# Kernel tuning notes

Hardware: AMD Instinct MI355X
Metric: run time of the kernel (lower is better)

The kernel has to match this reference:

```python
import jax, jax.numpy as jnp
import numpy as np


def setup_inputs() -> dict:
    key = jax.random.key(0)
    k_x, k_w, k_b = jax.random.split(key, 3)
    B, Cin, H, W = 32, 256, 56, 56
    Cout, KH, KW = 256, 3, 3
    x = jax.random.normal(k_x, (B, Cin, H, W), dtype=jnp.float32)
    fp_weight = jax.random.normal(k_w, (Cout, Cin, KH, KW), dtype=jnp.float32)
    # binary quantization, conv_mode='input_ch': per-output-channel scale
    scaling_factors = jnp.mean(jnp.abs(fp_weight), axis=(1, 2, 3), keepdims=True)  # [Cout,1,1,1]
    quant_weights = jnp.sign(fp_weight)  # values in {-1,0,1}
    bias = jax.random.normal(k_b, (Cout,), dtype=jnp.float32)
    return {"x": x, "scaling_factors": scaling_factors,
            "quant_weights": quant_weights, "bias": bias}


def reference(x, scaling_factors, quant_weights, bias):
    # Dequantize: per-out-channel scale times sign weights
    new_weights = scaling_factors * quant_weights  # [Cout,Cin,3,3]
    out = jax.lax.conv_general_dilated(
        x, new_weights,
        window_strides=(1, 1),
        padding=((1, 1), (1, 1)),
        dimension_numbers=("NCHW", "OIHW", "NCHW"),
    )
    return out + bias[None, :, None, None]
```

## Files before the change

### kernel.cpp

```cpp
#include <hip/hip_runtime.h>

using half8   = __attribute__((ext_vector_type(8))) _Float16;
using floatx4 = __attribute__((ext_vector_type(4))) float;
using floatx2 = __attribute__((ext_vector_type(2))) float;
using short8  = __attribute__((ext_vector_type(8))) short;

__global__ void repack_weights(const float* __restrict__ qw,
                               _Float16* __restrict__ wre, int n) {
  int t = blockIdx.x * 256 + threadIdx.x;
  if (t >= n) return;
  int c = t & 255, co = (t >> 8) & 255, s = t >> 16;
  wre[t] = (_Float16)qw[(co * 256 + c) * 9 + s];
}

__global__ __launch_bounds__(256, 2) void binconv_fused(
    const float* __restrict__ x, const float* __restrict__ scale,
    const float* __restrict__ bias, const _Float16* __restrict__ wre,
    float* __restrict__ out)
{
  __shared__ _Float16 xs[2 * 4 * 64 * 40];

  const int tid  = threadIdx.x;
  const int nb   = blockIdx.x;
  const int b    = nb / 28;
  const int h0   = (nb % 28) * 2;
  const int wave = tid >> 6;
  const int lane = tid & 63;
  const int nl   = lane & 15;
  const int quad = lane >> 4;
  const int co_wave = wave * 64;

  {
    short8 z = {0, 0, 0, 0, 0, 0, 0, 0};
    short8* xs8 = reinterpret_cast<short8*>(xs);
#pragma unroll
    for (int i = 0; i < 10; ++i) xs8[tid + i * 256] = z;
  }

  const int p   = lane & 15;
  const int wq  = lane >> 4;
  const int w0  = wq * 14;
  const int h   = h0 + wave - 1;
  const bool hok = (h >= 0) && (h < 56);
  const float* xca = x + (((size_t)b * 256 + 2 * p) * 56 + (hok ? h : 0)) * 56 + w0;
  const float* xcb = xca + 3136;
  _Float16* const wrow = xs + wave * 2560 + 2 * p;

  floatx2 va[7], vb[7];

  int bbase[7];
#pragma unroll
  for (int j = 0; j < 7; ++j) {
    int n = j * 16 + nl;
    int r = (n >= 56) ? 1 : 0;
    int w = n - r * 56;
    bbase[j] = (r * 64 + w) * 80 + quad * 16;
  }

  const _Float16* aptr[4];
#pragma unroll
  for (int mi = 0; mi < 4; ++mi)
    aptr[mi] = wre + (co_wave + mi * 16 + nl) * 256 + quad * 8;

  floatx4 acc[4][7];
#pragma unroll
  for (int mi = 0; mi < 4; ++mi)
#pragma unroll
    for (int j = 0; j < 7; ++j)
      acc[mi][j] = (floatx4){0.f, 0.f, 0.f, 0.f};

  __syncthreads();

  if (hok) {
#pragma unroll
    for (int i = 0; i < 7; ++i) {
      va[i] = *reinterpret_cast<const floatx2*>(xca + 2 * i);
      vb[i] = *reinterpret_cast<const floatx2*>(xcb + 2 * i);
    }
#pragma unroll
    for (int i = 0; i < 7; ++i) {
      auto u = __builtin_amdgcn_cvt_pkrtz(va[i][0], vb[i][0]);
      auto v = __builtin_amdgcn_cvt_pkrtz(va[i][1], vb[i][1]);
      *reinterpret_cast<decltype(u)*>(wrow + (w0 + 2 * i + 1) * 40) = u;
      *reinterpret_cast<decltype(v)*>(wrow + (w0 + 2 * i + 2) * 40) = v;
    }
  }

  int bufe = 0;
  for (int cc = 0; cc < 8; ++cc) {
    __syncthreads();
    if (cc < 7 && hok) {
      const float* A = xca + (size_t)(cc + 1) * 100352;
      const float* B = xcb + (size_t)(cc + 1) * 100352;
#pragma unroll
      for (int i = 0; i < 7; ++i) {
        va[i] = *reinterpret_cast<const floatx2*>(A + 2 * i);
        vb[i] = *reinterpret_cast<const floatx2*>(B + 2 * i);
      }
    }
    const int c0 = cc * 32;
    const char* xb = reinterpret_cast<const char*>(xs) + bufe * 2;
#pragma unroll
    for (int s = 0; s < 9; ++s) {
      const int kh = s / 3, kw = s - kh * 3;
      half8 a[4];
#pragma unroll
      for (int mi = 0; mi < 4; ++mi)
        a[mi] = *reinterpret_cast<const half8*>(aptr[mi] + s * 65536 + c0);
      const int soff = (kh * 64 + kw) * 80;
#pragma unroll
      for (int j = 0; j < 7; ++j) {
        half8 bf = *reinterpret_cast<const half8*>(xb + bbase[j] + soff);
#pragma unroll
        for (int mi = 0; mi < 4; ++mi)
          acc[mi][j] = __builtin_amdgcn_mfma_f32_16x16x32_f16(a[mi], bf, acc[mi][j], 0, 0, 0);
      }
    }
    if (cc < 7 && hok) {
      _Float16* d = wrow + (bufe ^ 10240);
#pragma unroll
      for (int i = 0; i < 7; ++i) {
        auto u = __builtin_amdgcn_cvt_pkrtz(va[i][0], vb[i][0]);
        auto v = __builtin_amdgcn_cvt_pkrtz(va[i][1], vb[i][1]);
        *reinterpret_cast<decltype(u)*>(d + (w0 + 2 * i + 1) * 40) = u;
        *reinterpret_cast<decltype(v)*>(d + (w0 + 2 * i + 2) * 40) = v;
      }
    }
    bufe ^= 10240;
  }

#pragma unroll
  for (int mi = 0; mi < 4; ++mi) {
#pragma unroll
    for (int reg = 0; reg < 4; ++reg) {
      int co = co_wave + mi * 16 + quad * 4 + reg;
      float s_ = scale[co];
      float bi = bias[co];
#pragma unroll
      for (int j = 0; j < 7; ++j) {
        int n = j * 16 + nl;
        int r = (n >= 56) ? 1 : 0;
        int w = n - r * 56;
        out[(((size_t)b * 256 + co) * 56 + (h0 + r)) * 56 + w] =
            acc[mi][j][reg] * s_ + bi;
      }
    }
  }
}

extern "C" void kernel_launch(void* const* d_in, const int* in_sizes, int n_in,
                              void* d_out, int out_size, void* d_ws, size_t ws_size,
                              hipStream_t stream) {
  const float* x     = (const float*)d_in[0];
  const float* scale = (const float*)d_in[1];
  const float* qw    = (const float*)d_in[2];
  const float* bias  = (const float*)d_in[3];
  float* out = (float*)d_out;

  _Float16* wre = (_Float16*)d_ws;

  repack_weights<<<2304, 256, 0, stream>>>(qw, wre, 9 * 256 * 256);
  binconv_fused<<<896, 256, 0, stream>>>(x, scale, bias, wre, out);
}
```

Baseline: 335.0 us.

## Split output channels across eight waves per block and raise MFMA priority

Doubles the block to 512 threads so each wave computes 32 output channels instead of 64. This halves the accumulator registers per wave and aims for more waves per CU to hide latency. The input staging is remapped so each thread loads one channel and writes scalar fp16 values into LDS instead of packed pairs. It also wraps the MFMA loop in s_setprio to favour the compute phase. The trade-off is that weight fragments are now reloaded by twice as many waves, LDS stores are narrower, and there is more synchronisation per block.

```diff
diff --git a/kernel.cpp b/kernel.cpp
--- a/kernel.cpp
+++ b/kernel.cpp
@@ -13,7 +13,7 @@
   wre[t] = (_Float16)qw[(co * 256 + c) * 9 + s];
 }
 
-__global__ __launch_bounds__(256, 2) void binconv_fused(
+__global__ __launch_bounds__(512, 4) void binconv_fused(
     const float* __restrict__ x, const float* __restrict__ scale,
     const float* __restrict__ bias, const _Float16* __restrict__ wre,
     float* __restrict__ out)
@@ -28,43 +28,45 @@
   const int lane = tid & 63;
   const int nl   = lane & 15;
   const int quad = lane >> 4;
-  const int co_wave = wave * 64;
+  const int co_wave = wave * 32;
 
   {
     short8 z = {0, 0, 0, 0, 0, 0, 0, 0};
     short8* xs8 = reinterpret_cast<short8*>(xs);
 #pragma unroll
-    for (int i = 0; i < 10; ++i) xs8[tid + i * 256] = z;
+    for (int i = 0; i < 5; ++i) xs8[tid + i * 512] = z;
   }
 
-  const int p   = lane & 15;
-  const int wq  = lane >> 4;
-  const int w0  = wq * 14;
-  const int h   = h0 + wave - 1;
-  const bool hok = (h >= 0) && (h < 56);
-  const float* xca = x + (((size_t)b * 256 + 2 * p) * 56 + (hok ? h : 0)) * 56 + w0;
-  const float* xcb = xca + 3136;
-  _Float16* const wrow = xs + wave * 2560 + 2 * p;
+  const int r     = wave >> 1;
+  const int chalf = wave & 1;
+  const int sc    = lane & 15;
+  const int q     = lane >> 4;
+  const int ch    = chalf * 16 + sc;
+  const int w0    = q * 14;
+  const int h     = h0 + r - 1;
+  const bool hok  = (h >= 0) && (h < 56);
+  const float* xc = x + (((size_t)b * 256 + ch) * 56 + (hok ? h : 0)) * 56 + w0;
+  _Float16* const wrow = xs + r * 2560 + ch;
 
-  floatx2 va[7], vb[7];
+  floatx2 va[7];
 
   int bbase[7];
 #pragma unroll
   for (int j = 0; j < 7; ++j) {
     int n = j * 16 + nl;
-    int r = (n >= 56) ? 1 : 0;
-    int w = n - r * 56;
-    bbase[j] = (r * 64 + w) * 80 + quad * 16;
+    int rr = (n >= 56) ? 1 : 0;
+    int w = n - rr * 56;
+    bbase[j] = (rr * 64 + w) * 80 + quad * 16;
   }
 
-  const _Float16* aptr[4];
+  const _Float16* aptr[2];
 #pragma unroll
-  for (int mi = 0; mi < 4; ++mi)
+  for (int mi = 0; mi < 2; ++mi)
     aptr[mi] = wre + (co_wave + mi * 16 + nl) * 256 + quad * 8;
 
-  floatx4 acc[4][7];
+  floatx4 acc[2][7];
 #pragma unroll
-  for (int mi = 0; mi < 4; ++mi)
+  for (int mi = 0; mi < 2; ++mi)
 #pragma unroll
     for (int j = 0; j < 7; ++j)
       acc[mi][j] = (floatx4){0.f, 0.f, 0.f, 0.f};
@@ -73,16 +75,12 @@
 
   if (hok) {
 #pragma unroll
-    for (int i = 0; i < 7; ++i) {
-      va[i] = *reinterpret_cast<const floatx2*>(xca + 2 * i);
-      vb[i] = *reinterpret_cast<const floatx2*>(xcb + 2 * i);
-    }
+    for (int i = 0; i < 7; ++i)
+      va[i] = *reinterpret_cast<const floatx2*>(xc + 2 * i);
 #pragma unroll
     for (int i = 0; i < 7; ++i) {
-      auto u = __builtin_amdgcn_cvt_pkrtz(va[i][0], vb[i][0]);
-      auto v = __builtin_amdgcn_cvt_pkrtz(va[i][1], vb[i][1]);
-      *reinterpret_cast<decltype(u)*>(wrow + (w0 + 2 * i + 1) * 40) = u;
-      *reinterpret_cast<decltype(v)*>(wrow + (w0 + 2 * i + 2) * 40) = v;
+      wrow[(w0 + 2 * i + 1) * 40] = (_Float16)va[i][0];
+      wrow[(w0 + 2 * i + 2) * 40] = (_Float16)va[i][1];
     }
   }
 
@@ -90,47 +88,44 @@
   for (int cc = 0; cc < 8; ++cc) {
     __syncthreads();
     if (cc < 7 && hok) {
-      const float* A = xca + (size_t)(cc + 1) * 100352;
-      const float* B = xcb + (size_t)(cc + 1) * 100352;
+      const float* A = xc + (size_t)(cc + 1) * 100352;
 #pragma unroll
-      for (int i = 0; i < 7; ++i) {
+      for (int i = 0; i < 7; ++i)
         va[i] = *reinterpret_cast<const floatx2*>(A + 2 * i);
-        vb[i] = *reinterpret_cast<const floatx2*>(B + 2 * i);
-      }
     }
     const int c0 = cc * 32;
     const char* xb = reinterpret_cast<const char*>(xs) + bufe * 2;
+    __builtin_amdgcn_s_setprio(1);
 #pragma unroll
     for (int s = 0; s < 9; ++s) {
       const int kh = s / 3, kw = s - kh * 3;
-      half8 a[4];
+      half8 a[2];
 #pragma unroll
-      for (int mi = 0; mi < 4; ++mi)
+      for (int mi = 0; mi < 2; ++mi)
         a[mi] = *reinterpret_cast<const half8*>(aptr[mi] + s * 65536 + c0);
       const int soff = (kh * 64 + kw) * 80;
 #pragma unroll
       for (int j = 0; j < 7; ++j) {
         half8 bf = *reinterpret_cast<const half8*>(xb + bbase[j] + soff);
 #pragma unroll
-        for (int mi = 0; mi < 4; ++mi)
+        for (int mi = 0; mi < 2; ++mi)
           acc[mi][j] = __builtin_amdgcn_mfma_f32_16x16x32_f16(a[mi], bf, acc[mi][j], 0, 0, 0);
       }
     }
+    __builtin_amdgcn_s_setprio(0);
     if (cc < 7 && hok) {
       _Float16* d = wrow + (bufe ^ 10240);
 #pragma unroll
       for (int i = 0; i < 7; ++i) {
-        auto u = __builtin_amdgcn_cvt_pkrtz(va[i][0], vb[i][0]);
-        auto v = __builtin_amdgcn_cvt_pkrtz(va[i][1], vb[i][1]);
-        *reinterpret_cast<decltype(u)*>(d + (w0 + 2 * i + 1) * 40) = u;
-        *reinterpret_cast<decltype(v)*>(d + (w0 + 2 * i + 2) * 40) = v;
+        d[(w0 + 2 * i + 1) * 40] = (_Float16)va[i][0];
+        d[(w0 + 2 * i + 2) * 40] = (_Float16)va[i][1];
       }
     }
     bufe ^= 10240;
   }
 
 #pragma unroll
-  for (int mi = 0; mi < 4; ++mi) {
+  for (int mi = 0; mi < 2; ++mi) {
 #pragma unroll
     for (int reg = 0; reg < 4; ++reg) {
       int co = co_wave + mi * 16 + quad * 4 + reg;
@@ -139,9 +134,9 @@
 #pragma unroll
       for (int j = 0; j < 7; ++j) {
         int n = j * 16 + nl;
-        int r = (n >= 56) ? 1 : 0;
-        int w = n - r * 56;
-        out[(((size_t)b * 256 + co) * 56 + (h0 + r)) * 56 + w] =
+        int rr = (n >= 56) ? 1 : 0;
+        int w = n - rr * 56;
+        out[(((size_t)b * 256 + co) * 56 + (h0 + rr)) * 56 + w] =
             acc[mi][j][reg] * s_ + bi;
       }
     }
@@ -160,5 +155,5 @@
   _Float16* wre = (_Float16*)d_ws;
 
   repack_weights<<<2304, 256, 0, stream>>>(qw, wre, 9 * 256 * 256);
-  binconv_fused<<<896, 256, 0, stream>>>(x, scale, bias, wre, out);
+  binconv_fused<<<896, 512, 0, stream>>>(x, scale, bias, wre, out);
 }
```

Result: faster. 323.0 us (-3.6%).

## Restage input tile per-lane-column with split prefetch and MFMA priority

Applied to the files above, without the earlier changes.

Changes the global-to-LDS staging so each lane loads one spatial column across 32 channels (scalar coalesced loads across lanes) and writes 16-half vectors to LDS, instead of 2-channel packed pairs per lane. The prefetch of the next channel chunk is split into two halves interleaved between the first 5 and last 4 kernel taps, and s_setprio raises wave priority around the MFMA blocks. The intent is better overlap of global loads and LDS writes with matrix work and fewer, wider LDS stores. It increases register pressure with 32 staged floats per lane and may change LDS bank conflict behaviour.

```diff
diff --git a/kernel.cpp b/kernel.cpp
--- a/kernel.cpp
+++ b/kernel.cpp
@@ -1,9 +1,10 @@
 #include <hip/hip_runtime.h>
 
 using half8   = __attribute__((ext_vector_type(8))) _Float16;
+using half2v  = __attribute__((ext_vector_type(2))) _Float16;
 using floatx4 = __attribute__((ext_vector_type(4))) float;
-using floatx2 = __attribute__((ext_vector_type(2))) float;
 using short8  = __attribute__((ext_vector_type(8))) short;
+using uint4v  = __attribute__((ext_vector_type(4))) unsigned int;
 
 __global__ void repack_weights(const float* __restrict__ qw,
                                _Float16* __restrict__ wre, int n) {
@@ -13,7 +14,19 @@
   wre[t] = (_Float16)qw[(co * 256 + c) * 9 + s];
 }
 
-__global__ __launch_bounds__(256, 2) void binconv_fused(
+__device__ __forceinline__ void store16(_Float16* d, const float* sv) {
+  unsigned int u[8];
+#pragma unroll
+  for (int i = 0; i < 8; ++i)
+    u[i] = __builtin_bit_cast(unsigned int,
+             __builtin_amdgcn_cvt_pkrtz(sv[2 * i], sv[2 * i + 1]));
+  uint4v v0 = {u[0], u[1], u[2], u[3]};
+  uint4v v1 = {u[4], u[5], u[6], u[7]};
+  *reinterpret_cast<uint4v*>(d)     = v0;
+  *reinterpret_cast<uint4v*>(d + 8) = v1;
+}
+
+__global__ __launch_bounds__(256, 2) void binconv_v6(
     const float* __restrict__ x, const float* __restrict__ scale,
     const float* __restrict__ bias, const _Float16* __restrict__ wre,
     float* __restrict__ out)
@@ -37,16 +50,10 @@
     for (int i = 0; i < 10; ++i) xs8[tid + i * 256] = z;
   }
 
-  const int p   = lane & 15;
-  const int wq  = lane >> 4;
-  const int w0  = wq * 14;
-  const int h   = h0 + wave - 1;
-  const bool hok = (h >= 0) && (h < 56);
-  const float* xca = x + (((size_t)b * 256 + 2 * p) * 56 + (hok ? h : 0)) * 56 + w0;
-  const float* xcb = xca + 3136;
-  _Float16* const wrow = xs + wave * 2560 + 2 * p;
-
-  floatx2 va[7], vb[7];
+  const int h    = h0 + wave - 1;
+  const bool sok = (h >= 0) && (h < 56) && (lane < 56);
+  const float* xrow = x + (((size_t)b * 256) * 56 + (sok ? h : 0)) * 56 + lane;
+  const int wofs = wave * 2560 + (1 + lane) * 40;
 
   int bbase[7];
 #pragma unroll
@@ -71,37 +78,31 @@
 
   __syncthreads();
 
-  if (hok) {
+  float s0[16], s1[16];
+  if (sok) {
 #pragma unroll
-    for (int i = 0; i < 7; ++i) {
-      va[i] = *reinterpret_cast<const floatx2*>(xca + 2 * i);
-      vb[i] = *reinterpret_cast<const floatx2*>(xcb + 2 * i);
-    }
+    for (int ci = 0; ci < 16; ++ci) s0[ci] = xrow[ci * 3136];
 #pragma unroll
-    for (int i = 0; i < 7; ++i) {
-      auto u = __builtin_amdgcn_cvt_pkrtz(va[i][0], vb[i][0]);
-      auto v = __builtin_amdgcn_cvt_pkrtz(va[i][1], vb[i][1]);
-      *reinterpret_cast<decltype(u)*>(wrow + (w0 + 2 * i + 1) * 40) = u;
-      *reinterpret_cast<decltype(v)*>(wrow + (w0 + 2 * i + 2) * 40) = v;
-    }
+    for (int ci = 0; ci < 16; ++ci) s1[ci] = xrow[(16 + ci) * 3136];
+    store16(xs + wofs, s0);
+    store16(xs + wofs + 16, s1);
   }
 
-  int bufe = 0;
+  int bufel = 0;
   for (int cc = 0; cc < 8; ++cc) {
     __syncthreads();
-    if (cc < 7 && hok) {
-      const float* A = xca + (size_t)(cc + 1) * 100352;
-      const float* B = xcb + (size_t)(cc + 1) * 100352;
+    const float* xn = xrow + (size_t)(cc + 1) * 32 * 3136;
+    if (cc < 7 && sok) {
 #pragma unroll
-      for (int i = 0; i < 7; ++i) {
-        va[i] = *reinterpret_cast<const floatx2*>(A + 2 * i);
-        vb[i] = *reinterpret_cast<const floatx2*>(B + 2 * i);
-      }
+      for (int ci = 0; ci < 16; ++ci) s0[ci] = xn[ci * 3136];
     }
     const int c0 = cc * 32;
-    const char* xb = reinterpret_cast<const char*>(xs) + bufe * 2;
+    const char* xb = (const char*)xs + bufel * 2;
+    _Float16* const wd = xs + (bufel ^ 10240) + wofs;
+
+    __builtin_amdgcn_s_setprio(1);
 #pragma unroll
-    for (int s = 0; s < 9; ++s) {
+    for (int s = 0; s < 5; ++s) {
       const int kh = s / 3, kw = s - kh * 3;
       half8 a[4];
 #pragma unroll
@@ -116,17 +117,32 @@
           acc[mi][j] = __builtin_amdgcn_mfma_f32_16x16x32_f16(a[mi], bf, acc[mi][j], 0, 0, 0);
       }
     }
-    if (cc < 7 && hok) {
-      _Float16* d = wrow + (bufe ^ 10240);
+    __builtin_amdgcn_s_setprio(0);
+    if (cc < 7 && sok) {
+      store16(wd, s0);
 #pragma unroll
-      for (int i = 0; i < 7; ++i) {
-        auto u = __builtin_amdgcn_cvt_pkrtz(va[i][0], vb[i][0]);
-        auto v = __builtin_amdgcn_cvt_pkrtz(va[i][1], vb[i][1]);
-        *reinterpret_cast<decltype(u)*>(d + (w0 + 2 * i + 1) * 40) = u;
-        *reinterpret_cast<decltype(v)*>(d + (w0 + 2 * i + 2) * 40) = v;
+      for (int ci = 0; ci < 16; ++ci) s1[ci] = xn[(16 + ci) * 3136];
+    }
+    __builtin_amdgcn_s_setprio(1);
+#pragma unroll
+    for (int s = 5; s < 9; ++s) {
+      const int kh = s / 3, kw = s - kh * 3;
+      half8 a[4];
+#pragma unroll
+      for (int mi = 0; mi < 4; ++mi)
+        a[mi] = *reinterpret_cast<const half8*>(aptr[mi] + s * 65536 + c0);
+      const int soff = (kh * 64 + kw) * 80;
+#pragma unroll
+      for (int j = 0; j < 7; ++j) {
+        half8 bf = *reinterpret_cast<const half8*>(xb + bbase[j] + soff);
+#pragma unroll
+        for (int mi = 0; mi < 4; ++mi)
+          acc[mi][j] = __builtin_amdgcn_mfma_f32_16x16x32_f16(a[mi], bf, acc[mi][j], 0, 0, 0);
       }
     }
-    bufe ^= 10240;
+    __builtin_amdgcn_s_setprio(0);
+    if (cc < 7 && sok) store16(wd + 16, s1);
+    bufel ^= 10240;
   }
 
 #pragma unroll
@@ -160,5 +176,5 @@
   _Float16* wre = (_Float16*)d_ws;
 
   repack_weights<<<2304, 256, 0, stream>>>(qw, wre, 9 * 256 * 256);
-  binconv_fused<<<896, 256, 0, stream>>>(x, scale, bias, wre, out);
+  binconv_v6<<<896, 256, 0, stream>>>(x, scale, bias, wre, out);
 }
```

New measurement: 319.9 us. 1.05x faster.
